# Kernel optimization log

Hardware: AMD Instinct MI355X
Metric: run time of the kernel (lower is better)

## Reference

```python
import jax, jax.numpy as jnp
import numpy as np

B, H, S, D = 2, 12, 4096, 64

def setup_inputs() -> dict:
    key = jax.random.key(0)
    kq, kk, kv = jax.random.split(key, 3)
    Q = jax.random.normal(kq, (B, H, S, D), dtype=jnp.float32)
    K = jax.random.normal(kk, (B, H, S, D), dtype=jnp.float32)
    V = jax.random.normal(kv, (B, H, S, D), dtype=jnp.float32)
    attn_mask = jnp.zeros((1, 1, 1, 1), dtype=bool)  # unused by the original forward
    return {"Q": Q, "K": K, "V": V, "attn_mask": attn_mask}

def reference(Q, K, V, attn_mask):
    d_k = K.shape[3]
    # scores: [B, H, S, S] -- naive full materialization, matching the original
    scores = jnp.einsum("bhqd,bhkd->bhqk", Q, K) / np.sqrt(d_k).astype(Q.dtype)
    attn = jax.nn.softmax(scores, axis=-1)
    context = jnp.einsum("bhqk,bhkd->bhqd", attn, V)
    return context
```

## Files before the change

### kernel.cpp

```cpp
#include <hip/hip_runtime.h>

typedef _Float16 half4_t __attribute__((ext_vector_type(4)));
typedef _Float16 half8_t __attribute__((ext_vector_type(8)));
typedef __fp16  fp16x2_t __attribute__((ext_vector_type(2)));
typedef float floatx4 __attribute__((ext_vector_type(4)));

constexpr int S_  = 4096;
constexpr int D_  = 64;
constexpr int NBH = 24;
constexpr int BM  = 128;
constexpr int BN  = 64;
constexpr float SC2 = 0.125f * 1.44269504088896340736f;

__global__ __launch_bounds__(256) void preconv(
    const float* __restrict__ K, const float* __restrict__ V,
    _Float16* __restrict__ Kh, _Float16* __restrict__ Vh)
{
  __shared__ float tile[64 * 68];
  const int kt = blockIdx.x, bh = blockIdx.y, tid = threadIdx.x;
  const size_t tbase = ((size_t)bh * 64 + kt) * 4096;
#pragma unroll
  for (int it = 0; it < 2; ++it) {
    size_t i = tbase + (size_t)(tid + 256 * it) * 8;
    float4 a = *(const float4*)(K + i);
    float4 b = *(const float4*)(K + i + 4);
    *(half8_t*)(Kh + i) = (half8_t){
      (_Float16)(a.x*SC2),(_Float16)(a.y*SC2),(_Float16)(a.z*SC2),(_Float16)(a.w*SC2),
      (_Float16)(b.x*SC2),(_Float16)(b.y*SC2),(_Float16)(b.z*SC2),(_Float16)(b.w*SC2) };
  }
#pragma unroll
  for (int it = 0; it < 4; ++it) {
    int r  = (tid >> 4) + 16 * it;
    int c4 = (tid & 15) * 4;
    *(float4*)(&tile[r * 68 + c4]) = *(const float4*)(V + tbase + (size_t)r * 64 + c4);
  }
  __syncthreads();
  const int d = tid >> 2;
  _Float16 out[16];
#pragma unroll
  for (int j = 0; j < 16; ++j) {
    int key = 32 * (j >> 3) + 16 * ((j >> 2) & 1) + 4 * (tid & 3) + (j & 3);
    out[j] = (_Float16)tile[key * 68 + d];
  }
  _Float16* dst = Vh + tbase + (size_t)d * 64 + (tid & 3) * 16;
  *(half8_t*)(dst)     = *(half8_t*)(&out[0]);
  *(half8_t*)(dst + 8) = *(half8_t*)(&out[8]);
}


__device__ __forceinline__ void async16(const _Float16* g, _Float16* l) {
  __builtin_amdgcn_global_load_lds((const __attribute__((address_space(1))) void*)g,
                                   (__attribute__((address_space(3))) void*)l, 16, 0, 0);
}

__global__ __launch_bounds__(512, 4) void fattn2(
    const float* __restrict__ Qf, const _Float16* __restrict__ Kh,
    const _Float16* __restrict__ Vh, float* __restrict__ O)
{
  __shared__ __align__(16) _Float16 smem[8 * 4096];

  const int tid  = threadIdx.x;
  const int lane = tid & 63;
  const int w    = tid >> 6;
  const int g    = lane >> 4;
  const int m    = lane & 15;
  const int qh   = w & 3;
  const int kh2  = w >> 2;

  const int bid  = blockIdx.x;
  const int xcd  = bid & 7;
  const int slot = bid >> 3;
  const int bh   = xcd * 3 + (slot >> 5);
  const int qblk = slot & 31;
  const size_t base = (size_t)bh * S_ * D_;
  const int q0g = qblk * BM + qh * 32;

  half8_t qf[2][2];
#pragma unroll
  for (int qt = 0; qt < 2; ++qt)
#pragma unroll
    for (int ks = 0; ks < 2; ++ks) {
      const float4* qp = (const float4*)(Qf + base + (size_t)(q0g + qt*16 + m) * D_ + 8*g + 32*ks);
      float4 a = qp[0], b = qp[1];
      qf[qt][ks] = (half8_t){ (_Float16)a.x,(_Float16)a.y,(_Float16)a.z,(_Float16)a.w,
                              (_Float16)b.x,(_Float16)b.y,(_Float16)b.z,(_Float16)b.w };
    }

  floatx4 oacc[2][4];
#pragma unroll
  for (int qt = 0; qt < 2; ++qt)
#pragma unroll
    for (int db = 0; db < 4; ++db) oacc[qt][db] = (floatx4){0.f,0.f,0.f,0.f};
  floatx4 lacc[2];
  lacc[0] = (floatx4){0.f,0.f,0.f,0.f};
  lacc[1] = (floatx4){0.f,0.f,0.f,0.f};
  const half8_t vones = (half8_t){ (_Float16)1.f,(_Float16)1.f,(_Float16)1.f,(_Float16)1.f,
                                   (_Float16)1.f,(_Float16)1.f,(_Float16)1.f,(_Float16)1.f };

  const int goff0 = (tid >> 3) * 64 + (((tid & 7) ^ ((tid >> 3) & 7)) << 3);
  const int l0 = w * 512;

  const _Float16* Kb = Kh + base;
  const _Float16* Vb = Vh + base;

  _Float16 *kr0 = smem,           *kr1 = smem + 4096;
  _Float16 *kw0 = smem + 8192,    *kw1 = smem + 12288;
  _Float16 *vr0 = smem + 16384,   *vr1 = smem + 20480;
  _Float16 *vw0 = smem + 24576,   *vw1 = smem + 28672;

  auto stage = [&](_Float16* kd, _Float16* vd, int kt) {
    const _Float16* Kt = Kb + ((size_t)kt << 12);
    const _Float16* Vt = Vb + ((size_t)kt << 12);
    async16(Kt + goff0, kd + l0);
    async16(Vt + goff0, vd + l0);
  };

  const int r7 = m & 7;
  const int krow = 32 * kh2 + m;

  auto compute = [&](const _Float16* kbuf, const _Float16* vbuf) {
    half8_t kf[2][2];
#pragma unroll
    for (int nb2 = 0; nb2 < 2; ++nb2) {
      kf[nb2][0] = *(const half8_t*)(&kbuf[(krow + 16*nb2) * 64 + ((g    ) ^ r7) * 8]);
      kf[nb2][1] = *(const half8_t*)(&kbuf[(krow + 16*nb2) * 64 + ((g + 4) ^ r7) * 8]);
    }
    half8_t vf[4];
#pragma unroll
    for (int db = 0; db < 4; ++db)
      vf[db] = *(const half8_t*)(&vbuf[(16*db + m) * 64 + ((2*g + kh2) ^ r7) * 8]);

#pragma unroll
    for (int qt = 0; qt < 2; ++qt) {
      floatx4 s0 = (floatx4){0.f,0.f,0.f,0.f};
      floatx4 s1 = (floatx4){0.f,0.f,0.f,0.f};
      s0 = __builtin_amdgcn_mfma_f32_16x16x32_f16(kf[0][0], qf[qt][0], s0, 0, 0, 0);
      s0 = __builtin_amdgcn_mfma_f32_16x16x32_f16(kf[0][1], qf[qt][1], s0, 0, 0, 0);
      s1 = __builtin_amdgcn_mfma_f32_16x16x32_f16(kf[1][0], qf[qt][0], s1, 0, 0, 0);
      s1 = __builtin_amdgcn_mfma_f32_16x16x32_f16(kf[1][1], qf[qt][1], s1, 0, 0, 0);

      float p0 = __builtin_amdgcn_exp2f(s0[0]);
      float p1 = __builtin_amdgcn_exp2f(s0[1]);
      float p2 = __builtin_amdgcn_exp2f(s0[2]);
      float p3 = __builtin_amdgcn_exp2f(s0[3]);
      float p4 = __builtin_amdgcn_exp2f(s1[0]);
      float p5 = __builtin_amdgcn_exp2f(s1[1]);
      float p6 = __builtin_amdgcn_exp2f(s1[2]);
      float p7 = __builtin_amdgcn_exp2f(s1[3]);

      union { half8_t h8; fp16x2_t h2[4]; } pu;
      pu.h2[0] = __builtin_amdgcn_cvt_pkrtz(p0, p1);
      pu.h2[1] = __builtin_amdgcn_cvt_pkrtz(p2, p3);
      pu.h2[2] = __builtin_amdgcn_cvt_pkrtz(p4, p5);
      pu.h2[3] = __builtin_amdgcn_cvt_pkrtz(p6, p7);

      lacc[qt] = __builtin_amdgcn_mfma_f32_16x16x32_f16(pu.h8, vones, lacc[qt], 0, 0, 0);

#pragma unroll
      for (int db = 0; db < 4; ++db)
        oacc[qt][db] = __builtin_amdgcn_mfma_f32_16x16x32_f16(pu.h8, vf[db], oacc[qt][db], 0, 0, 0);
    }
  };

  stage(kr0, vr0, 0);
  stage(kr1, vr1, 1);

  for (int it = 0; it < 32; ++it) {
    asm volatile("s_waitcnt vmcnt(0)\n\ts_barrier" ::: "memory");
    stage(kw0, vw0, (2*it + 2) & 63);
    stage(kw1, vw1, (2*it + 3) & 63);

    compute(kr0, vr0);
    compute(kr1, vr1);

    _Float16* t;
    t = kr0; kr0 = kw0; kw0 = t;
    t = kr1; kr1 = kw1; kw1 = t;
    t = vr0; vr0 = vw0; vw0 = t;
    t = vr1; vr1 = vw1; vw1 = t;
  }

  __syncthreads();
  float* red  = (float*)smem;
  float* lred = red + 10240;
  const int ro = qh * 2560;

  if (kh2 == 1) {
#pragma unroll
    for (int qt = 0; qt < 2; ++qt) {
#pragma unroll
      for (int db = 0; db < 4; ++db)
        *(floatx4*)(&red[ro + (16*db + m) * 40 + qt*16 + 4*g]) = oacc[qt][db];
      if (m == 0) {
#pragma unroll
        for (int r = 0; r < 4; ++r)
          lred[qh * 32 + qt*16 + 4*g + r] = lacc[qt][r];
      }
    }
  }
  __syncthreads();
  if (kh2 == 0) {
#pragma unroll
    for (int qt = 0; qt < 2; ++qt) {
      floatx4 linv;
#pragma unroll
      for (int r = 0; r < 4; ++r)
        linv[r] = 1.0f / (lacc[qt][r] + lred[qh * 32 + qt*16 + 4*g + r]);
      float* Op = O + base + (size_t)(q0g + qt*16) * D_;
#pragma unroll
      for (int db = 0; db < 4; ++db) {
        floatx4 part = *(const floatx4*)(&red[ro + (16*db + m) * 40 + qt*16 + 4*g]);
        floatx4 o = oacc[qt][db] + part;
#pragma unroll
        for (int r = 0; r < 4; ++r)
          Op[(size_t)(4*g + r) * D_ + 16*db + m] = o[r] * linv[r];
      }
    }
  }
}

constexpr int SKf = 72;
constexpr int SVf = 68;
__global__ __launch_bounds__(256, 3) void fattn_fb(
    const float* __restrict__ Q, const float* __restrict__ K,
    const float* __restrict__ V, float* __restrict__ O)
{
  __shared__ __align__(16) _Float16 Ks[2][64 * SKf];
  __shared__ __align__(16) _Float16 Vs[2][64 * SVf];
  const int tid = threadIdx.x, lane = tid & 63, w = tid >> 6, g = lane >> 4, m = lane & 15;
  const int bid = blockIdx.x, xcd = bid & 7, slot = bid >> 3;
  const int bh = xcd * 3 + (slot >> 5), qblk = slot & 31;
  const size_t base = (size_t)bh * S_ * D_;
  const int q0 = qblk * BM + w * 32;
  half8_t qf[2][2];
#pragma unroll
  for (int qt = 0; qt < 2; ++qt)
#pragma unroll
    for (int ks = 0; ks < 2; ++ks) {
      const float4* qp = (const float4*)(Q + base + (size_t)(q0 + qt*16 + m) * D_ + 8*g + 32*ks);
      float4 a = qp[0], b = qp[1];
      qf[qt][ks] = (half8_t){ (_Float16)(a.x*SC2),(_Float16)(a.y*SC2),(_Float16)(a.z*SC2),(_Float16)(a.w*SC2),
                              (_Float16)(b.x*SC2),(_Float16)(b.y*SC2),(_Float16)(b.z*SC2),(_Float16)(b.w*SC2) };
    }
  floatx4 oacc[2][4];
#pragma unroll
  for (int qt = 0; qt < 2; ++qt)
#pragma unroll
    for (int db = 0; db < 4; ++db) oacc[qt][db] = (floatx4){0.f,0.f,0.f,0.f};
  float lsum[2] = {0.f, 0.f};
  const float* Kb = K + base; const float* Vb = V + base;
  float4 kreg[4]; float vreg[16];
  const int sL = ((lane >> 2) ^ (lane >> 4)) & 3;
  auto issue = [&](int kt) {
    const float* Kt = Kb + (size_t)kt * BN * D_;
#pragma unroll
    for (int it = 0; it < 2; ++it) {
      int sl = tid + 256*it; int key = sl >> 3; int c8 = (sl & 7) << 3;
      const float4* p = (const float4*)(Kt + (size_t)key * D_ + c8);
      kreg[2*it] = p[0]; kreg[2*it+1] = p[1];
    }
    const float* Vt = Vb + (size_t)kt * BN * D_;
#pragma unroll
    for (int it = 0; it < 4; ++it) {
      int kb = it * 16 + (w << 2);
      const float* vp = Vt + (size_t)kb * D_ + lane;
      vreg[4*it+0]=vp[0]; vreg[4*it+1]=vp[D_]; vreg[4*it+2]=vp[2*D_]; vreg[4*it+3]=vp[3*D_];
    }
  };
  auto commit = [&](int buf) {
    _Float16* Kd = Ks[buf]; _Float16* Vd = Vs[buf];
#pragma unroll
    for (int it = 0; it < 2; ++it) {
      int sl = tid + 256*it; int key = sl >> 3; int c8 = (sl & 7) << 3;
      float4 a = kreg[2*it], b = kreg[2*it+1];
      *(half8_t*)(&Kd[key * SKf + c8]) = (half8_t){ (_Float16)a.x,(_Float16)a.y,(_Float16)a.z,(_Float16)a.w,
                                                    (_Float16)b.x,(_Float16)b.y,(_Float16)b.z,(_Float16)b.w };
    }
#pragma unroll
    for (int it = 0; it < 4; ++it)
      *(half4_t*)(&Vd[lane * SVf + 4 * ((4*it + w) ^ sL)]) =
        (half4_t){ (_Float16)vreg[4*it+0], (_Float16)vreg[4*it+1], (_Float16)vreg[4*it+2], (_Float16)vreg[4*it+3] };
  };
  issue(0); commit(0); __syncthreads();
  const int s0i = m >> 2;
  for (int kt = 0; kt < 64; ++kt) {
    const int cur = kt & 1;
    if (kt < 63) issue(kt + 1);
    const _Float16* Kd = Ks[cur]; const _Float16* Vd = Vs[cur];
    half8_t kf[4][2];
#pragma unroll
    for (int nb = 0; nb < 4; ++nb) {
      kf[nb][0] = *(const half8_t*)(&Kd[(16*nb + m) * SKf + 8*g]);
      kf[nb][1] = *(const half8_t*)(&Kd[(16*nb + m) * SKf + 8*g + 32]);
    }
    half4_t vf[4][4];
#pragma unroll
    for (int nb = 0; nb < 4; ++nb)
#pragma unroll
      for (int db = 0; db < 4; ++db)
        vf[nb][db] = *(const half4_t*)(&Vd[(16*db + m) * SVf + 4 * ((4*nb + g) ^ s0i ^ db)]);
#pragma unroll
    for (int qt = 0; qt < 2; ++qt) {
      floatx4 sacc[4];
#pragma unroll
      for (int nb = 0; nb < 4; ++nb) {
        floatx4 acc = (floatx4){0.f,0.f,0.f,0.f};
        acc = __builtin_amdgcn_mfma_f32_16x16x32_f16(kf[nb][0], qf[qt][0], acc, 0, 0, 0);
        acc = __builtin_amdgcn_mfma_f32_16x16x32_f16(kf[nb][1], qf[qt][1], acc, 0, 0, 0);
        sacc[nb] = acc;
      }
      half4_t pf[4]; float ls = 0.f;
#pragma unroll
      for (int nb = 0; nb < 4; ++nb) {
        float p0 = __builtin_amdgcn_exp2f(sacc[nb][0]); float p1 = __builtin_amdgcn_exp2f(sacc[nb][1]);
        float p2 = __builtin_amdgcn_exp2f(sacc[nb][2]); float p3 = __builtin_amdgcn_exp2f(sacc[nb][3]);
        ls += p0 + p1 + p2 + p3;
        pf[nb] = (half4_t){ (_Float16)p0, (_Float16)p1, (_Float16)p2, (_Float16)p3 };
      }
      lsum[qt] += ls;
#pragma unroll
      for (int nb = 0; nb < 4; ++nb)
#pragma unroll
        for (int db = 0; db < 4; ++db)
          oacc[qt][db] = __builtin_amdgcn_mfma_f32_16x16x16f16(pf[nb], vf[nb][db], oacc[qt][db], 0, 0, 0);
    }
    if (kt < 63) commit(1 - cur);
    __syncthreads();
  }
#pragma unroll
  for (int qt = 0; qt < 2; ++qt) {
    float l = lsum[qt];
    l += __shfl_xor(l, 16); l += __shfl_xor(l, 32);
    floatx4 linv;
#pragma unroll
    for (int r = 0; r < 4; ++r) linv[r] = 1.0f / __shfl(l, (lane & 48) + 4*g + r);
    float* Op = O + base + (size_t)(q0 + qt*16) * D_;
#pragma unroll
    for (int db = 0; db < 4; ++db)
#pragma unroll
      for (int r = 0; r < 4; ++r)
        Op[(size_t)(4*g + r) * D_ + 16*db + m] = oacc[qt][db][r] * linv[r];
  }
}

extern "C" void kernel_launch(void* const* d_in, const int* in_sizes, int n_in,
                              void* d_out, int out_size, void* d_ws, size_t ws_size,
                              hipStream_t stream) {
  const float* Q = (const float*)d_in[0];
  const float* K = (const float*)d_in[1];
  const float* V = (const float*)d_in[2];
  float* Out = (float*)d_out;

  constexpr size_t NELEM = (size_t)NBH * S_ * D_;
  constexpr size_t NEED  = 2 * NELEM * sizeof(_Float16);

  if (ws_size >= NEED) {
    _Float16* Khp = (_Float16*)d_ws;
    _Float16* Vhp = Khp + NELEM;
    preconv<<<dim3(64, NBH), 256, 0, stream>>>(K, V, Khp, Vhp);
    fattn2<<<NBH * (S_ / BM), 512, 0, stream>>>(Q, Khp, Vhp, Out);
  } else {
    fattn_fb<<<NBH * (S_ / BM), 256, 0, stream>>>(Q, K, V, Out);
  }
}
```

Before: 213.6 us.

## Specialize warps into QK/exp producers and PV consumers via LDS P buffers

Replaces the split-K scheme, where all 8 warps did QK, exp and PV on half the keys and then reduced, with warp specialization. Warps 0-3 compute scores and exp into a swizzled P tile in shared memory. Warps 4-7 consume P against V to accumulate output and the row sum, pipelined one tile behind with double-buffered K, V and P. This removes the final cross-warp reduction and is meant to overlap exp work with MFMA. In exchange it adds P round-trips through LDS, two barriers per tile, and uneven load between the two warp groups.

```diff
diff --git a/kernel.cpp b/kernel.cpp
--- a/kernel.cpp
+++ b/kernel.cpp
@@ -53,19 +53,19 @@
                                    (__attribute__((address_space(3))) void*)l, 16, 0, 0);
 }
 
-__global__ __launch_bounds__(512, 4) void fattn2(
+__global__ __launch_bounds__(512, 4) void fattn3(
     const float* __restrict__ Qf, const _Float16* __restrict__ Kh,
     const _Float16* __restrict__ Vh, float* __restrict__ O)
 {
-  __shared__ __align__(16) _Float16 smem[8 * 4096];
+  __shared__ __align__(16) _Float16 smem[32768];
 
   const int tid  = threadIdx.x;
   const int lane = tid & 63;
   const int w    = tid >> 6;
   const int g    = lane >> 4;
   const int m    = lane & 15;
+  const bool isQK = (w < 4);
   const int qh   = w & 3;
-  const int kh2  = w >> 2;
 
   const int bid  = blockIdx.x;
   const int xcd  = bid & 7;
@@ -75,25 +75,28 @@
   const size_t base = (size_t)bh * S_ * D_;
   const int q0g = qblk * BM + qh * 32;
 
+  const int r7 = m & 7;
+
   half8_t qf[2][2];
-#pragma unroll
-  for (int qt = 0; qt < 2; ++qt)
-#pragma unroll
-    for (int ks = 0; ks < 2; ++ks) {
-      const float4* qp = (const float4*)(Qf + base + (size_t)(q0g + qt*16 + m) * D_ + 8*g + 32*ks);
-      float4 a = qp[0], b = qp[1];
-      qf[qt][ks] = (half8_t){ (_Float16)a.x,(_Float16)a.y,(_Float16)a.z,(_Float16)a.w,
-                              (_Float16)b.x,(_Float16)b.y,(_Float16)b.z,(_Float16)b.w };
-    }
-
+  if (isQK) {
+#pragma unroll
+    for (int qt = 0; qt < 2; ++qt)
+#pragma unroll
+      for (int ks = 0; ks < 2; ++ks) {
+        const float4* qp = (const float4*)(Qf + base + (size_t)(q0g + qt*16 + m) * D_ + 8*g + 32*ks);
+        float4 a = qp[0], b = qp[1];
+        qf[qt][ks] = (half8_t){ (_Float16)a.x,(_Float16)a.y,(_Float16)a.z,(_Float16)a.w,
+                                (_Float16)b.x,(_Float16)b.y,(_Float16)b.z,(_Float16)b.w };
+      }
+  }
   floatx4 oacc[2][4];
-#pragma unroll
-  for (int qt = 0; qt < 2; ++qt)
+  floatx4 lacc[2];
+#pragma unroll
+  for (int qt = 0; qt < 2; ++qt) {
+    lacc[qt] = (floatx4){0.f,0.f,0.f,0.f};
 #pragma unroll
     for (int db = 0; db < 4; ++db) oacc[qt][db] = (floatx4){0.f,0.f,0.f,0.f};
-  floatx4 lacc[2];
-  lacc[0] = (floatx4){0.f,0.f,0.f,0.f};
-  lacc[1] = (floatx4){0.f,0.f,0.f,0.f};
+  }
   const half8_t vones = (half8_t){ (_Float16)1.f,(_Float16)1.f,(_Float16)1.f,(_Float16)1.f,
                                    (_Float16)1.f,(_Float16)1.f,(_Float16)1.f,(_Float16)1.f };
 
@@ -103,118 +106,104 @@
   const _Float16* Kb = Kh + base;
   const _Float16* Vb = Vh + base;
 
-  _Float16 *kr0 = smem,           *kr1 = smem + 4096;
-  _Float16 *kw0 = smem + 8192,    *kw1 = smem + 12288;
-  _Float16 *vr0 = smem + 16384,   *vr1 = smem + 20480;
-  _Float16 *vw0 = smem + 24576,   *vw1 = smem + 28672;
-
-  auto stage = [&](_Float16* kd, _Float16* vd, int kt) {
-    const _Float16* Kt = Kb + ((size_t)kt << 12);
-    const _Float16* Vt = Vb + ((size_t)kt << 12);
-    async16(Kt + goff0, kd + l0);
-    async16(Vt + goff0, vd + l0);
-  };
-
-  const int r7 = m & 7;
-  const int krow = 32 * kh2 + m;
-
-  auto compute = [&](const _Float16* kbuf, const _Float16* vbuf) {
-    half8_t kf[2][2];
-#pragma unroll
-    for (int nb2 = 0; nb2 < 2; ++nb2) {
-      kf[nb2][0] = *(const half8_t*)(&kbuf[(krow + 16*nb2) * 64 + ((g    ) ^ r7) * 8]);
-      kf[nb2][1] = *(const half8_t*)(&kbuf[(krow + 16*nb2) * 64 + ((g + 4) ^ r7) * 8]);
-    }
-    half8_t vf[4];
-#pragma unroll
-    for (int db = 0; db < 4; ++db)
-      vf[db] = *(const half8_t*)(&vbuf[(16*db + m) * 64 + ((2*g + kh2) ^ r7) * 8]);
-
+  _Float16* const K0 = smem;
+  _Float16* const K1 = smem + 4096;
+  _Float16* const V0 = smem + 8192;
+  _Float16* const V1 = smem + 12288;
+  _Float16* const P0 = smem + 16384;
+  _Float16* const P1 = smem + 24576;
+
+  auto stageK = [&](int kt, _Float16* kd) {
+    async16(Kb + (((size_t)(kt & 63)) << 12) + goff0, kd + l0);
+  };
+  auto stageV = [&](int kt, _Float16* vd) {
+    async16(Vb + (((size_t)kt) << 12) + goff0, vd + l0);
+  };
+
+  auto produce = [&](const _Float16* kbuf, _Float16* pbuf) {
 #pragma unroll
     for (int qt = 0; qt < 2; ++qt) {
-      floatx4 s0 = (floatx4){0.f,0.f,0.f,0.f};
-      floatx4 s1 = (floatx4){0.f,0.f,0.f,0.f};
-      s0 = __builtin_amdgcn_mfma_f32_16x16x32_f16(kf[0][0], qf[qt][0], s0, 0, 0, 0);
-      s0 = __builtin_amdgcn_mfma_f32_16x16x32_f16(kf[0][1], qf[qt][1], s0, 0, 0, 0);
-      s1 = __builtin_amdgcn_mfma_f32_16x16x32_f16(kf[1][0], qf[qt][0], s1, 0, 0, 0);
-      s1 = __builtin_amdgcn_mfma_f32_16x16x32_f16(kf[1][1], qf[qt][1], s1, 0, 0, 0);
-
-      float p0 = __builtin_amdgcn_exp2f(s0[0]);
-      float p1 = __builtin_amdgcn_exp2f(s0[1]);
-      float p2 = __builtin_amdgcn_exp2f(s0[2]);
-      float p3 = __builtin_amdgcn_exp2f(s0[3]);
-      float p4 = __builtin_amdgcn_exp2f(s1[0]);
-      float p5 = __builtin_amdgcn_exp2f(s1[1]);
-      float p6 = __builtin_amdgcn_exp2f(s1[2]);
-      float p7 = __builtin_amdgcn_exp2f(s1[3]);
-
-      union { half8_t h8; fp16x2_t h2[4]; } pu;
-      pu.h2[0] = __builtin_amdgcn_cvt_pkrtz(p0, p1);
-      pu.h2[1] = __builtin_amdgcn_cvt_pkrtz(p2, p3);
-      pu.h2[2] = __builtin_amdgcn_cvt_pkrtz(p4, p5);
-      pu.h2[3] = __builtin_amdgcn_cvt_pkrtz(p6, p7);
-
-      lacc[qt] = __builtin_amdgcn_mfma_f32_16x16x32_f16(pu.h8, vones, lacc[qt], 0, 0, 0);
-
-#pragma unroll
-      for (int db = 0; db < 4; ++db)
-        oacc[qt][db] = __builtin_amdgcn_mfma_f32_16x16x32_f16(pu.h8, vf[db], oacc[qt][db], 0, 0, 0);
-    }
-  };
-
-  stage(kr0, vr0, 0);
-  stage(kr1, vr1, 1);
-
-  for (int it = 0; it < 32; ++it) {
-    asm volatile("s_waitcnt vmcnt(0)\n\ts_barrier" ::: "memory");
-    stage(kw0, vw0, (2*it + 2) & 63);
-    stage(kw1, vw1, (2*it + 3) & 63);
-
-    compute(kr0, vr0);
-    compute(kr1, vr1);
-
-    _Float16* t;
-    t = kr0; kr0 = kw0; kw0 = t;
-    t = kr1; kr1 = kw1; kw1 = t;
-    t = vr0; vr0 = vw0; vw0 = t;
-    t = vr1; vr1 = vw1; vw1 = t;
-  }
-
-  __syncthreads();
-  float* red  = (float*)smem;
-  float* lred = red + 10240;
-  const int ro = qh * 2560;
-
-  if (kh2 == 1) {
+#pragma unroll
+      for (int h = 0; h < 2; ++h) {
+        const _Float16* kr = kbuf + (32*h + m) * 64;
+        half8_t kf00 = *(const half8_t*)(kr + ((g    ) ^ r7) * 8);
+        half8_t kf01 = *(const half8_t*)(kr + ((g + 4) ^ r7) * 8);
+        half8_t kf10 = *(const half8_t*)(kr + 16*64 + ((g    ) ^ r7) * 8);
+        half8_t kf11 = *(const half8_t*)(kr + 16*64 + ((g + 4) ^ r7) * 8);
+        floatx4 s0 = (floatx4){0.f,0.f,0.f,0.f};
+        floatx4 s1 = (floatx4){0.f,0.f,0.f,0.f};
+        s0 = __builtin_amdgcn_mfma_f32_16x16x32_f16(kf00, qf[qt][0], s0, 0, 0, 0);
+        s0 = __builtin_amdgcn_mfma_f32_16x16x32_f16(kf01, qf[qt][1], s0, 0, 0, 0);
+        s1 = __builtin_amdgcn_mfma_f32_16x16x32_f16(kf10, qf[qt][0], s1, 0, 0, 0);
+        s1 = __builtin_amdgcn_mfma_f32_16x16x32_f16(kf11, qf[qt][1], s1, 0, 0, 0);
+
+        float p0 = __builtin_amdgcn_exp2f(s0[0]);
+        float p1 = __builtin_amdgcn_exp2f(s0[1]);
+        float p2 = __builtin_amdgcn_exp2f(s0[2]);
+        float p3 = __builtin_amdgcn_exp2f(s0[3]);
+        float p4 = __builtin_amdgcn_exp2f(s1[0]);
+        float p5 = __builtin_amdgcn_exp2f(s1[1]);
+        float p6 = __builtin_amdgcn_exp2f(s1[2]);
+        float p7 = __builtin_amdgcn_exp2f(s1[3]);
+
+        union { half8_t h8; fp16x2_t h2[4]; } pu;
+        pu.h2[0] = __builtin_amdgcn_cvt_pkrtz(p0, p1);
+        pu.h2[1] = __builtin_amdgcn_cvt_pkrtz(p2, p3);
+        pu.h2[2] = __builtin_amdgcn_cvt_pkrtz(p4, p5);
+        pu.h2[3] = __builtin_amdgcn_cvt_pkrtz(p6, p7);
+
+        *(half8_t*)(pbuf + (qh*32 + qt*16 + m) * 64 + ((32*h + 8*g) ^ (r7 << 3))) = pu.h8;
+      }
+    }
+  };
+
+  auto consume = [&](const _Float16* pbuf, const _Float16* vbuf) {
 #pragma unroll
     for (int qt = 0; qt < 2; ++qt) {
 #pragma unroll
-      for (int db = 0; db < 4; ++db)
-        *(floatx4*)(&red[ro + (16*db + m) * 40 + qt*16 + 4*g]) = oacc[qt][db];
-      if (m == 0) {
-#pragma unroll
-        for (int r = 0; r < 4; ++r)
-          lred[qh * 32 + qt*16 + 4*g + r] = lacc[qt][r];
-      }
-    }
-  }
-  __syncthreads();
-  if (kh2 == 0) {
+      for (int h = 0; h < 2; ++h) {
+        half8_t pa = *(const half8_t*)(pbuf + (qh*32 + qt*16 + m) * 64 + ((32*h + 8*g) ^ (r7 << 3)));
+        lacc[qt] = __builtin_amdgcn_mfma_f32_16x16x32_f16(pa, vones, lacc[qt], 0, 0, 0);
+#pragma unroll
+        for (int db = 0; db < 4; ++db) {
+          half8_t v8 = *(const half8_t*)(vbuf + (16*db + m) * 64 + ((2*g + h) ^ r7) * 8);
+          oacc[qt][db] = __builtin_amdgcn_mfma_f32_16x16x32_f16(pa, v8, oacc[qt][db], 0, 0, 0);
+        }
+      }
+    }
+  };
+
+  stageK(0, K0);
+
+  for (int t2 = 0; t2 < 32; ++t2) {
+    asm volatile("s_waitcnt vmcnt(0) lgkmcnt(0)\n\ts_barrier" ::: "memory");
+    stageK(2*t2 + 1, K1);
+    stageV(2*t2,     V0);
+    if (isQK)           produce(K0, P0);
+    else if (t2 > 0)    consume(P1, V1);
+
+    asm volatile("s_waitcnt vmcnt(0) lgkmcnt(0)\n\ts_barrier" ::: "memory");
+    stageK(2*t2 + 2, K0);
+    stageV(2*t2 + 1, V1);
+    if (isQK)  produce(K1, P1);
+    else       consume(P0, V0);
+  }
+  asm volatile("s_waitcnt vmcnt(0) lgkmcnt(0)\n\ts_barrier" ::: "memory");
+  if (!isQK) consume(P1, V1);
+
+  if (!isQK) {
 #pragma unroll
     for (int qt = 0; qt < 2; ++qt) {
       floatx4 linv;
 #pragma unroll
       for (int r = 0; r < 4; ++r)
-        linv[r] = 1.0f / (lacc[qt][r] + lred[qh * 32 + qt*16 + 4*g + r]);
+        linv[r] = 1.0f / lacc[qt][r];
       float* Op = O + base + (size_t)(q0g + qt*16) * D_;
 #pragma unroll
-      for (int db = 0; db < 4; ++db) {
-        floatx4 part = *(const floatx4*)(&red[ro + (16*db + m) * 40 + qt*16 + 4*g]);
-        floatx4 o = oacc[qt][db] + part;
+      for (int db = 0; db < 4; ++db)
 #pragma unroll
         for (int r = 0; r < 4; ++r)
-          Op[(size_t)(4*g + r) * D_ + 16*db + m] = o[r] * linv[r];
-      }
+          Op[(size_t)(4*g + r) * D_ + 16*db + m] = oacc[qt][db][r] * linv[r];
     }
   }
 }
@@ -358,7 +347,7 @@
     _Float16* Khp = (_Float16*)d_ws;
     _Float16* Vhp = Khp + NELEM;
     preconv<<<dim3(64, NBH), 256, 0, stream>>>(K, V, Khp, Vhp);
-    fattn2<<<NBH * (S_ / BM), 512, 0, stream>>>(Q, Khp, Vhp, Out);
+    fattn3<<<NBH * (S_ / BM), 512, 0, stream>>>(Q, Khp, Vhp, Out);
   } else {
     fattn_fb<<<NBH * (S_ / BM), 256, 0, stream>>>(Q, K, V, Out);
   }
```

Result: no change. 212.8 us (-0.4%).
